# Performance work log

Hardware: AMD Instinct MI355X
Metric: run time of the kernel (lower is better)

The kernel has to match this reference:

```python
import jax, jax.numpy as jnp
import numpy as np

G = 20000   # total_genes = nodes per graph = output dim
HID = 64    # hidden_channels
H = 4       # attention heads (concat=False -> mean over heads)
E = 640000  # edges (avg degree 32)
B = 128     # batch of cell-line samples
PD = 600    # perturbation feature dim
NEG_SLOPE = 0.2


def _gat(x, edge_index, W, a_src, a_dst, b, heads):
    """PyG GATConv with add_self_loops=True, concat=False (head mean)."""
    N = x.shape[0]
    C = W.shape[1] // heads
    h = (x @ W).reshape(N, heads, C)              # [N,H,C]
    loop = jnp.arange(N, dtype=edge_index.dtype)
    src = jnp.concatenate([edge_index[0], loop])  # [E+N]
    dst = jnp.concatenate([edge_index[1], loop])
    e_src = jnp.sum(h * a_src[None], axis=-1)     # [N,H]
    e_dst = jnp.sum(h * a_dst[None], axis=-1)
    e = jax.nn.leaky_relu(e_src[src] + e_dst[dst], NEG_SLOPE)  # [E+N,H]
    # segment softmax over incoming edges of each target node
    m = jax.ops.segment_max(e, dst, num_segments=N)
    ex = jnp.exp(e - m[dst])
    denom = jax.ops.segment_sum(ex, dst, num_segments=N)
    alpha = ex / denom[dst]                        # [E+N,H]
    out = jax.ops.segment_sum(h[src] * alpha[:, :, None], dst, num_segments=N)
    return out.mean(axis=1) + b                    # concat=False -> mean heads


def _mlp(x, W1, b1, W2, b2):
    # MLP([a,b,c], 'Sigmoid'): Linear -> Sigmoid -> Linear (last act dropped)
    return jax.nn.sigmoid(x @ W1 + b1) @ W2 + b2


def setup_inputs() -> dict:
    key = jax.random.key(0)
    ks = jax.random.split(key, 26)
    s = 0.05  # small init to keep sigmoids in their active range
    rn = lambda k, shp: jax.random.normal(k, shp, jnp.float32)
    return {
        "x": rn(ks[0], (G, 1)),
        "edge_index": jax.random.randint(ks[1], (2, E), 0, G, dtype=jnp.int32),
        "pos": jnp.arange(G, dtype=jnp.int32),
        "ctrl": rn(ks[2], (B, G)),
        "pert": rn(ks[3], (B, PD)),
        "gene_embed": rn(ks[4], (G, HID)) * s,
        "conv1_W": rn(ks[5], (1 + HID, H * HID)) * s,
        "conv1_as": rn(ks[6], (H, HID)) * s,
        "conv1_ad": rn(ks[7], (H, HID)) * s,
        "conv1_b": rn(ks[8], (HID,)) * s,
        "lin1_W": rn(ks[9], (1 + HID, HID)) * s,
        "lin1_b": rn(ks[10], (HID,)) * s,
        "conv2_W": rn(ks[11], (HID, H * 1)) * s,
        "conv2_as": rn(ks[12], (H, 1)) * s,
        "conv2_ad": rn(ks[13], (H, 1)) * s,
        "conv2_b": rn(ks[14], (1,)) * s,
        "lin2_W": rn(ks[15], (HID, 1)) * s,
        "lin2_b": rn(ks[16], (1,)) * s,
        "pert_W1": rn(ks[17], (PD, 128)) * s,
        "pert_b1": rn(ks[18], (128,)) * s,
        "pert_W2": rn(ks[19], (128, HID)) * s,
        "pert_b2": rn(ks[20], (HID,)) * s,
        "pred_W1": rn(ks[21], (G + HID, 1024)) * s,
        "pred_b1": rn(ks[22], (1024,)) * s,
        "pred_W2": rn(ks[23], (1024, G)) * s,
        "pred_b2": rn(ks[24], (G,)) * s,
    }


def reference(x, edge_index, pos, ctrl, pert, gene_embed,
              conv1_W, conv1_as, conv1_ad, conv1_b, lin1_W, lin1_b,
              conv2_W, conv2_as, conv2_ad, conv2_b, lin2_W, lin2_b,
              pert_W1, pert_b1, pert_W2, pert_b2,
              pred_W1, pred_b1, pred_W2, pred_b2):
    # per-graph GNN (single cell-type key), all_feat=True
    xc = jnp.concatenate([x, gene_embed[pos]], axis=1)         # [G, 1+HID]
    h1 = jax.nn.sigmoid(_gat(xc, edge_index, conv1_W, conv1_as, conv1_ad, conv1_b, H)
                        + xc @ lin1_W + lin1_b)                # [G, HID]
    h2 = jax.nn.sigmoid(_gat(h1, edge_index, conv2_W, conv2_as, conv2_ad, conv2_b, H)
                        + h1 @ lin2_W + lin2_b)                # [G, 1]
    feat = h2[:, 0]                                            # dense batch squeeze -> [G]
    # every sample in the batch uses this cell type's features
    z = feat[None, :] + ctrl                                   # [B, G]
    p = _mlp(pert, pert_W1, pert_b1, pert_W2, pert_b2)         # embd_pert -> [B, HID]
    inp = jnp.concatenate([z, p], axis=1)                      # [B, G+HID]
    return _mlp(inp, pred_W1, pred_b1, pred_W2, pred_b2)       # [B, G]
```

## Files before the change

kernel.cpp:

```cpp
#include <hip/hip_runtime.h>
#include <math.h>

#define G 20000
#define E_EDGES 640000
#define HID 64
#define NHEAD 4
#define BATCH 128
#define PD 600
#define NEG 0.2f
#define MAXN 128

#define KA1 20096
#define NSTEP1 628
#define KSPLIT1 32
#define KA2 1024

#define ROWS_HC 16

typedef float v4f __attribute__((ext_vector_type(4)));
typedef short short8 __attribute__((ext_vector_type(8)));

__device__ __forceinline__ float sigmoidf_(float x){ return 1.0f/(1.0f+__expf(-x)); }
__device__ __forceinline__ float leakyf_(float x){ return x>=0.f ? x : NEG*x; }
__device__ __forceinline__ unsigned short f2bf(float f){
    unsigned int u = __float_as_uint(f);
    return (unsigned short)((u + 0x7FFFu + ((u >> 16) & 1u)) >> 16);
}
__device__ __forceinline__ float bf2f(unsigned short b){
    return __uint_as_float(((unsigned int)b) << 16);
}

__global__ __launch_bounds__(320)
void k_hc(const float* __restrict__ x, const int* __restrict__ pos,
          const float* __restrict__ ge, const float* __restrict__ Wc,
          const float* __restrict__ Wl, const float* __restrict__ as_,
          const float* __restrict__ ad_,
          unsigned short* __restrict__ hcb, float* __restrict__ hlin,
          float* __restrict__ es, float* __restrict__ ed)
{
    int t = threadIdx.x;
    int rb = blockIdx.x * ROWS_HC;
    __shared__ float xc[ROWS_HC][68];
    for (int l = t; l < ROWS_HC*65; l += 320){
        int r = l / 65, k = l - r*65;
        int row = rb + r;
        float v = 0.f;
        if (row < G) v = (k == 0) ? x[row] : ge[pos[row]*HID + (k-1)];
        xc[r][k] = v;
    }
    float wcol[65];
    if (t < 256){
        #pragma unroll
        for (int k = 0; k < 65; ++k) wcol[k] = Wc[k*256 + t];
    } else {
        int c = t - 256;
        #pragma unroll
        for (int k = 0; k < 65; ++k) wcol[k] = Wl[k*64 + c];
    }
    float a_s = 0.f, a_d = 0.f;
    if (t < 256){ a_s = as_[t]; a_d = ad_[t]; }
    __syncthreads();

    int nrow = G - rb; if (nrow > ROWS_HC) nrow = ROWS_HC;
    for (int r = 0; r < nrow; ++r){
        int row = rb + r;
        const float4* xr = (const float4*)&xc[r][0];
        float b0 = 0.f, b1 = 0.f, b2 = 0.f, b3 = 0.f;
        #pragma unroll
        for (int k4 = 0; k4 < 16; ++k4){
            float4 v = xr[k4];
            b0 += v.x*wcol[4*k4];
            b1 += v.y*wcol[4*k4+1];
            b2 += v.z*wcol[4*k4+2];
            b3 += v.w*wcol[4*k4+3];
        }
        float acc = (b0 + b1) + (b2 + b3) + xc[r][64] * wcol[64];
        if (t < 256){
            hcb[(size_t)row*256 + t] = f2bf(acc);
            float v1 = acc * a_s, v2 = acc * a_d;
            #pragma unroll
            for (int m = 32; m; m >>= 1){ v1 += __shfl_xor(v1, m); v2 += __shfl_xor(v2, m); }
            if ((t & 63) == 0){ int h = t >> 6; es[row*4+h] = v1; ed[row*4+h] = v2; }
        } else {
            hlin[(size_t)row*64 + (t - 256)] = acc;
        }
    }
}

__global__ void k_hist(const int* __restrict__ ei, int* __restrict__ cnt){
    int e = blockIdx.x*blockDim.x + threadIdx.x;
    if (e < E_EDGES) atomicAdd(&cnt[ei[E_EDGES + e]], 1);
}
__global__ void k_scan(const int* __restrict__ cnt, int* __restrict__ offs,
                       int* __restrict__ cur)
{
    __shared__ int ts[1024];
    int t = threadIdx.x;
    int base = t * 20;
    int loc[20];
    int s = 0;
    #pragma unroll
    for (int j = 0; j < 20; ++j){
        int i = base + j;
        int v = (i < G) ? cnt[i] : 0;
        loc[j] = s; s += v;
    }
    ts[t] = s;
    __syncthreads();
    for (int off = 1; off < 1024; off <<= 1){
        int add = (t >= off) ? ts[t - off] : 0;
        __syncthreads();
        ts[t] += add;
        __syncthreads();
    }
    int tb = (t == 0) ? 0 : ts[t - 1];
    #pragma unroll
    for (int j = 0; j < 20; ++j){
        int i = base + j;
        if (i < G){ int o = tb + loc[j]; offs[i] = o; cur[i] = o; }
    }
    if (t == 0) offs[G] = ts[1023];
}
__global__ void k_scatter(const int* __restrict__ ei, int* __restrict__ cur, int* __restrict__ csr){
    int e = blockIdx.x*blockDim.x + threadIdx.x;
    if (e < E_EDGES){
        int d = ei[E_EDGES + e];
        int p = atomicAdd(&cur[d], 1);
        csr[p] = ei[e];
    }
}

__global__ __launch_bounds__(256)
void k_gat1(const unsigned short* __restrict__ hcb, const float* __restrict__ hlin,
            const float* __restrict__ es, const float* __restrict__ ed,
            const int* __restrict__ offs, const int* __restrict__ csr,
            const float* __restrict__ bc1, const float* __restrict__ bl1,
            const float* __restrict__ W2c, const float* __restrict__ as2,
            const float* __restrict__ ad2, const float* __restrict__ Wl2,
            float* __restrict__ hh2, float* __restrict__ es2o,
            float* __restrict__ ed2o, float* __restrict__ lv)
{
    int t = threadIdx.x;
    int lane = t & 63, wv = t >> 6;
    int d = blockIdx.x * 4 + wv;
    __shared__ float4 wcache[4][MAXN];
    __shared__ int    wsrc[4][MAXN];
    int o = offs[d];
    int deg = offs[d+1] - o;
    int total = deg + 1;
    if (total > MAXN) total = MAXN;
    float4 edv = *(const float4*)(ed + d*4);

    float s0x=-1e30f, s0y=-1e30f, s0z=-1e30f, s0w=-1e30f;
    float s1x=-1e30f, s1y=-1e30f, s1z=-1e30f, s1w=-1e30f;
    if (lane < total){
        int s = (lane < deg) ? csr[o + lane] : d;
        wsrc[wv][lane] = s;
        float4 ev = *(const float4*)(es + s*4);
        s0x = leakyf_(ev.x + edv.x); s0y = leakyf_(ev.y + edv.y);
        s0z = leakyf_(ev.z + edv.z); s0w = leakyf_(ev.w + edv.w);
    }
    int i1 = lane + 64;
    if (i1 < total){
        int s = (i1 < deg) ? csr[o + i1] : d;
        wsrc[wv][i1] = s;
        float4 ev = *(const float4*)(es + s*4);
        s1x = leakyf_(ev.x + edv.x); s1y = leakyf_(ev.y + edv.y);
        s1z = leakyf_(ev.z + edv.z); s1w = leakyf_(ev.w + edv.w);
    }
    float m0 = fmaxf(s0x, s1x), m1 = fmaxf(s0y, s1y);
    float m2 = fmaxf(s0z, s1z), m3 = fmaxf(s0w, s1w);
    #pragma unroll
    for (int m = 32; m; m >>= 1){
        m0 = fmaxf(m0, __shfl_xor(m0, m)); m1 = fmaxf(m1, __shfl_xor(m1, m));
        m2 = fmaxf(m2, __shfl_xor(m2, m)); m3 = fmaxf(m3, __shfl_xor(m3, m));
    }
    float e0x = __expf(s0x - m0), e0y = __expf(s0y - m1);
    float e0z = __expf(s0z - m2), e0w = __expf(s0w - m3);
    float e1x = __expf(s1x - m0), e1y = __expf(s1y - m1);
    float e1z = __expf(s1z - m2), e1w = __expf(s1w - m3);
    float q0 = e0x + e1x, q1 = e0y + e1y, q2 = e0z + e1z, q3 = e0w + e1w;
    #pragma unroll
    for (int m = 32; m; m >>= 1){
        q0 += __shfl_xor(q0, m); q1 += __shfl_xor(q1, m);
        q2 += __shfl_xor(q2, m); q3 += __shfl_xor(q3, m);
    }
    float inv0 = 1.0f/q0, inv1 = 1.0f/q1, inv2 = 1.0f/q2, inv3 = 1.0f/q3;
    if (lane < total) wcache[wv][lane] = make_float4(e0x*inv0, e0y*inv1, e0z*inv2, e0w*inv3);
    if (i1   < total) wcache[wv][i1]   = make_float4(e1x*inv0, e1y*inv1, e1z*inv2, e1w*inv3);
    __syncthreads();

    int u = lane;
    int h = u >> 4;
    float a0=0.f, a1=0.f, a2=0.f, a3=0.f;
    uint2 v; float al;
    {
        int s = wsrc[wv][0];
        al = ((const float*)&wcache[wv][0])[h];
        v = *(const uint2*)(hcb + (size_t)s*256 + u*4);
    }
    for (int idx = 0; idx < total; ){
        uint2 vc = v; float ac = al;
        int nx = idx + 1;
        if (nx < total){
            int s2 = wsrc[wv][nx];
            al = ((const float*)&wcache[wv][nx])[h];
            v = *(const uint2*)(hcb + (size_t)s2*256 + u*4);
        }
        a0 += ac * __uint_as_float(vc.x << 16);
        a1 += ac * __uint_as_float(vc.x & 0xFFFF0000u);
        a2 += ac * __uint_as_float(vc.y << 16);
        a3 += ac * __uint_as_float(vc.y & 0xFFFF0000u);
        idx = nx;
    }
    a0 += __shfl_xor(a0, 16); a1 += __shfl_xor(a1, 16);
    a2 += __shfl_xor(a2, 16); a3 += __shfl_xor(a3, 16);
    a0 += __shfl_xor(a0, 32); a1 += __shfl_xor(a1, 32);
    a2 += __shfl_xor(a2, 32); a3 += __shfl_xor(a3, 32);

    int cb = (lane & 15) * 4;
    float4 hl  = *(const float4*)(hlin + (size_t)d*64 + cb);
    float4 bcv = *(const float4*)(bc1 + cb);
    float4 blv = *(const float4*)(bl1 + cb);
    float h0 = sigmoidf_(0.25f*a0 + bcv.x + hl.x + blv.x);
    float h1v= sigmoidf_(0.25f*a1 + bcv.y + hl.y + blv.y);
    float h2v= sigmoidf_(0.25f*a2 + bcv.z + hl.z + blv.z);
    float h3v= sigmoidf_(0.25f*a3 + bcv.w + hl.w + blv.w);
    float p0 = h0*W2c[cb*4+0] + h1v*W2c[(cb+1)*4+0] + h2v*W2c[(cb+2)*4+0] + h3v*W2c[(cb+3)*4+0];
    float p1 = h0*W2c[cb*4+1] + h1v*W2c[(cb+1)*4+1] + h2v*W2c[(cb+2)*4+1] + h3v*W2c[(cb+3)*4+1];
    float p2 = h0*W2c[cb*4+2] + h1v*W2c[(cb+1)*4+2] + h2v*W2c[(cb+2)*4+2] + h3v*W2c[(cb+3)*4+2];
    float p3 = h0*W2c[cb*4+3] + h1v*W2c[(cb+1)*4+3] + h2v*W2c[(cb+2)*4+3] + h3v*W2c[(cb+3)*4+3];
    float pl = h0*Wl2[cb] + h1v*Wl2[cb+1] + h2v*Wl2[cb+2] + h3v*Wl2[cb+3];
    #pragma unroll
    for (int m = 1; m <= 8; m <<= 1){
        p0 += __shfl_xor(p0, m); p1 += __shfl_xor(p1, m);
        p2 += __shfl_xor(p2, m); p3 += __shfl_xor(p3, m);
        pl += __shfl_xor(pl, m);
    }
    if (lane == 0){
        hh2[d*4+0] = p0; hh2[d*4+1] = p1; hh2[d*4+2] = p2; hh2[d*4+3] = p3;
        es2o[d*4+0] = p0*as2[0]; es2o[d*4+1] = p1*as2[1];
        es2o[d*4+2] = p2*as2[2]; es2o[d*4+3] = p3*as2[3];
        ed2o[d*4+0] = p0*ad2[0]; ed2o[d*4+1] = p1*ad2[1];
        ed2o[d*4+2] = p2*ad2[2]; ed2o[d*4+3] = p3*ad2[3];
        lv[d] = pl;
    }
}

__global__ void k_gat2(const float* __restrict__ hh2, const float* __restrict__ es2,
                       const float* __restrict__ ed2, const int* __restrict__ offs,
                       const int* __restrict__ csr, const float* __restrict__ lv,
                       const float* __restrict__ bc2, const float* __restrict__ bl2,
                       float* __restrict__ feat)
{
    int d = blockIdx.x; int j = threadIdx.x;
    int o = offs[d];
    int deg = offs[d+1] - o;
    int total = deg + 1;
    float edst[4];
    #pragma unroll
    for (int h = 0; h < 4; ++h) edst[h] = ed2[d*4+h];
    float lmax[4] = {-1e30f,-1e30f,-1e30f,-1e30f};
    for (int idx = j; idx < total; idx += 64){
        int s = (idx < deg) ? csr[o + idx] : d;
        #pragma unroll
        for (int h = 0; h < 4; ++h)
            lmax[h] = fmaxf(lmax[h], leakyf_(es2[s*4+h] + edst[h]));
    }
    #pragma unroll
    for (int h = 0; h < 4; ++h)
        for (int m = 32; m; m >>= 1) lmax[h] = fmaxf(lmax[h], __shfl_xor(lmax[h], m));
    float lsum[4] = {0.f,0.f,0.f,0.f};
    float lnum[4] = {0.f,0.f,0.f,0.f};
    for (int idx = j; idx < total; idx += 64){
        int s = (idx < deg) ? csr[o + idx] : d;
        #pragma unroll
        for (int h = 0; h < 4; ++h){
            float e  = leakyf_(es2[s*4+h] + edst[h]);
            float ex = __expf(e - lmax[h]);
            lsum[h] += ex;
            lnum[h] += ex * hh2[s*4+h];
        }
    }
    #pragma unroll
    for (int h = 0; h < 4; ++h){
        for (int m = 32; m; m >>= 1){ lsum[h] += __shfl_xor(lsum[h], m); lnum[h] += __shfl_xor(lnum[h], m); }
    }
    if (j == 0){
        float sum = 0.f;
        #pragma unroll
        for (int h = 0; h < 4; ++h) sum += lnum[h] / lsum[h];
        feat[d] = sigmoidf_(0.25f*sum + bc2[0] + lv[d] + bl2[0]);
    }
}

__global__ void k_prepA(const float* __restrict__ ctrl, const float* __restrict__ feat,
                        unsigned short* __restrict__ Abf)
{
    int col = blockIdx.x*256 + threadIdx.x;
    int row = blockIdx.y;
    if (col < 20000)
        Abf[(size_t)row*KA1 + col] = f2bf(ctrl[(size_t)row*20000 + col] + feat[col]);
}

__global__ void k_pert(const float* __restrict__ pert, const float* __restrict__ W1,
                       const float* __restrict__ b1, const float* __restrict__ W2,
                       const float* __restrict__ b2, unsigned short* __restrict__ Abf)
{
    int r = blockIdx.x; int t = threadIdx.x;
    __shared__ float hid[128];
    float acc = 0.f;
    for (int k = 0; k < PD; ++k) acc += pert[r*PD + k] * W1[k*128 + t];
    hid[t] = sigmoidf_(acc + b1[t]);
    __syncthreads();
    if (t < 64){
        float a2 = 0.f;
        for (int k = 0; k < 128; ++k) a2 += hid[k] * W2[k*64 + t];
        Abf[(size_t)r*KA1 + 20000 + t] = f2bf(a2 + b2[t]);
    } else if (t < 96){
        Abf[(size_t)r*KA1 + 20000 + t] = 0;
    }
}

__global__ __launch_bounds__(256, 2)
void k_gemm1m(const unsigned short* __restrict__ Abf, const float* __restrict__ W1,
              float* __restrict__ part)
{
    int t = threadIdx.x;
    int lane = t & 63, wv = t >> 6;
    int lane16 = lane & 15, quad = lane >> 4, quad8 = quad * 8;
    int colbase = blockIdx.x * 64;
    int ks = blockIdx.y;
    int sbeg = (ks * NSTEP1) / KSPLIT1;
    int send = ((ks + 1) * NSTEP1) / KSPLIT1;
    int nsteps = send - sbeg;
    int kbeg = sbeg * 32;
    __shared__ unsigned short Bs[2][32*64];

    v4f acc[8];
    #pragma unroll
    for (int i = 0; i < 8; ++i) acc[i] = (v4f){0.f,0.f,0.f,0.f};

    int krow = t >> 3;
    int ng   = (t & 7) * 8;
    {
        int kg = kbeg + krow;
        short8 p;
        if (kg < 20064){
            float4 a = *(const float4*)(W1 + (size_t)kg*1024 + colbase + ng);
            float4 b = *(const float4*)(W1 + (size_t)kg*1024 + colbase + ng + 4);
            p[0]=(short)f2bf(a.x); p[1]=(short)f2bf(a.y); p[2]=(short)f2bf(a.z); p[3]=(short)f2bf(a.w);
            p[4]=(short)f2bf(b.x); p[5]=(short)f2bf(b.y); p[6]=(short)f2bf(b.z); p[7]=(short)f2bf(b.w);
        } else {
            p = (short8){0,0,0,0,0,0,0,0};
        }
        *(short8*)&Bs[0][krow*64 + ng] = p;
    }
    __syncthreads();

    int cur = 0;
    for (int s = 0; s < nsteps; ++s){
        int kg = kbeg + s*32;
        short8 bfrag;
        #pragma unroll
        for (int j = 0; j < 8; ++j)
            bfrag[j] = (short)Bs[cur][(quad8 + j)*64 + wv*16 + lane16];
        float w[8];
        bool more = (s + 1) < nsteps;
        if (more){
            int kn = kg + 32 + krow;
            if (kn < 20064){
                float4 a = *(const float4*)(W1 + (size_t)kn*1024 + colbase + ng);
                float4 b = *(const float4*)(W1 + (size_t)kn*1024 + colbase + ng + 4);
                w[0]=a.x; w[1]=a.y; w[2]=a.z; w[3]=a.w; w[4]=b.x; w[5]=b.y; w[6]=b.z; w[7]=b.w;
            } else {
                #pragma unroll
                for (int i = 0; i < 8; ++i) w[i] = 0.f;
            }
        }
        #pragma unroll
        for (int mt = 0; mt < 8; ++mt){
            short8 af = *(const short8*)(Abf + (size_t)(mt*16 + lane16)*KA1 + kg + quad8);
            acc[mt] = __builtin_amdgcn_mfma_f32_16x16x32_bf16(af, bfrag, acc[mt], 0, 0, 0);
        }
        if (more){
            short8 p;
            #pragma unroll
            for (int i = 0; i < 8; ++i) p[i] = (short)f2bf(w[i]);
            *(short8*)&Bs[cur^1][krow*64 + ng] = p;
        }
        __syncthreads();
        cur ^= 1;
    }
    float* dst = part + (size_t)ks * 131072;
    int col = colbase + wv*16 + lane16;
    #pragma unroll
    for (int mt = 0; mt < 8; ++mt)
        #pragma unroll
        for (int r = 0; r < 4; ++r)
            dst[(size_t)(mt*16 + quad*4 + r)*1024 + col] = acc[mt][r];
}

__global__ void k_reduce(const float* __restrict__ part, const float* __restrict__ b1,
                         unsigned short* __restrict__ hidbf)
{
    int row = blockIdx.x;
    int col = blockIdx.y*256 + threadIdx.x;
    float s = 0.f;
    #pragma unroll
    for (int ks = 0; ks < KSPLIT1; ++ks)
        s += part[(size_t)ks*131072 + (size_t)row*1024 + col];
    hidbf[(size_t)row*1024 + col] = f2bf(sigmoidf_(s + b1[col]));
}

__global__ __launch_bounds__(256, 2)
void k_gemm2m(const unsigned short* __restrict__ hidbf, const float* __restrict__ W2,
              const float* __restrict__ b2, float* __restrict__ out)
{
    int t = threadIdx.x;
    int lane = t & 63, wv = t >> 6;
    int lane16 = lane & 15, quad = lane >> 4, quad8 = quad * 8;
    int colbase = blockIdx.x * 64;
    int rbase   = blockIdx.y * 64;
    __shared__ unsigned short Bs[2][32*64];

    v4f acc[4];
    #pragma unroll
    for (int i = 0; i < 4; ++i) acc[i] = (v4f){0.f,0.f,0.f,0.f};

    int krow = t >> 3;
    int ng   = (t & 7) * 8;
    bool cv = (colbase + ng) < 20000;
    {
        short8 p = (short8){0,0,0,0,0,0,0,0};
        if (cv){
            float4 a = *(const float4*)(W2 + (size_t)krow*20000 + colbase + ng);
            float4 b = *(const float4*)(W2 + (size_t)krow*20000 + colbase + ng + 4);
            p[0]=(short)f2bf(a.x); p[1]=(short)f2bf(a.y); p[2]=(short)f2bf(a.z); p[3]=(short)f2bf(a.w);
            p[4]=(short)f2bf(b.x); p[5]=(short)f2bf(b.y); p[6]=(short)f2bf(b.z); p[7]=(short)f2bf(b.w);
        }
        *(short8*)&Bs[0][krow*64 + ng] = p;
    }
    __syncthreads();

    int cur = 0;
    for (int s = 0; s < 32; ++s){
        int kg = s*32;
        short8 bfrag;
        #pragma unroll
        for (int j = 0; j < 8; ++j)
            bfrag[j] = (short)Bs[cur][(quad8 + j)*64 + wv*16 + lane16];
        float w[8];
        bool more = s < 31;
        if (more){
            if (cv){
                int kn = kg + 32 + krow;
                float4 a = *(const float4*)(W2 + (size_t)kn*20000 + colbase + ng);
                float4 b = *(const float4*)(W2 + (size_t)kn*20000 + colbase + ng + 4);
                w[0]=a.x; w[1]=a.y; w[2]=a.z; w[3]=a.w; w[4]=b.x; w[5]=b.y; w[6]=b.z; w[7]=b.w;
            } else {
                #pragma unroll
                for (int i = 0; i < 8; ++i) w[i] = 0.f;
            }
        }
        #pragma unroll
        for (int mt = 0; mt < 4; ++mt){
            short8 af = *(const short8*)(hidbf + (size_t)(rbase + mt*16 + lane16)*KA2 + kg + quad8);
            acc[mt] = __builtin_amdgcn_mfma_f32_16x16x32_bf16(af, bfrag, acc[mt], 0, 0, 0);
        }
        if (more){
            short8 p;
            #pragma unroll
            for (int i = 0; i < 8; ++i) p[i] = (short)f2bf(w[i]);
            *(short8*)&Bs[cur^1][krow*64 + ng] = p;
        }
        __syncthreads();
        cur ^= 1;
    }
    int col = colbase + wv*16 + lane16;
    if (col < 20000){
        float bb = b2[col];
        #pragma unroll
        for (int mt = 0; mt < 4; ++mt)
            #pragma unroll
            for (int r = 0; r < 4; ++r)
                out[(size_t)(rbase + mt*16 + quad*4 + r)*20000 + col] = acc[mt][r] + bb;
    }
}

extern "C" void kernel_launch(void* const* d_in, const int* in_sizes, int n_in,
                              void* d_out, int out_size, void* d_ws, size_t ws_size,
                              hipStream_t stream)
{
    const float* x    = (const float*)d_in[0];
    const int*   ei   = (const int*)  d_in[1];
    const int*   pos  = (const int*)  d_in[2];
    const float* ctrl = (const float*)d_in[3];
    const float* pert = (const float*)d_in[4];
    const float* ge   = (const float*)d_in[5];
    const float* c1W  = (const float*)d_in[6];
    const float* c1as = (const float*)d_in[7];
    const float* c1ad = (const float*)d_in[8];
    const float* c1b  = (const float*)d_in[9];
    const float* l1W  = (const float*)d_in[10];
    const float* l1b  = (const float*)d_in[11];
    const float* c2W  = (const float*)d_in[12];
    const float* c2as = (const float*)d_in[13];
    const float* c2ad = (const float*)d_in[14];
    const float* c2b  = (const float*)d_in[15];
    const float* l2W  = (const float*)d_in[16];
    const float* l2b  = (const float*)d_in[17];
    const float* pW1  = (const float*)d_in[18];
    const float* pb1  = (const float*)d_in[19];
    const float* pW2  = (const float*)d_in[20];
    const float* pb2  = (const float*)d_in[21];
    const float* prW1 = (const float*)d_in[22];
    const float* prb1 = (const float*)d_in[23];
    const float* prW2 = (const float*)d_in[24];
    const float* prb2 = (const float*)d_in[25];
    float* out = (float*)d_out;

    char* ws = (char*)d_ws;
    size_t off = 0;
    auto alloc = [&](size_t bytes)->void*{
        void* pp = ws + off;
        off += (bytes + 255) & ~(size_t)255;
        return pp;
    };
    unsigned short* hcb  = (unsigned short*)alloc((size_t)G*256*2);
    float* hlin = (float*)alloc((size_t)G*64*4);
    float* es1  = (float*)alloc((size_t)G*4*4);
    float* ed1  = (float*)alloc((size_t)G*4*4);
    float* hh2  = (float*)alloc((size_t)G*4*4);
    float* es2  = (float*)alloc((size_t)G*4*4);
    float* ed2  = (float*)alloc((size_t)G*4*4);
    float* lv   = (float*)alloc((size_t)G*4);
    float* feat = (float*)alloc((size_t)G*4);
    unsigned short* hidbf = (unsigned short*)alloc((size_t)128*KA2*2);
    unsigned short* Abf1  = (unsigned short*)alloc((size_t)128*KA1*2);
    float* part = (float*)alloc((size_t)KSPLIT1*131072*4);
    int*   cnt  = (int*)alloc((size_t)G*4);
    int*   offs = (int*)alloc((size_t)(G+1)*4);
    int*   cur  = (int*)alloc((size_t)G*4);
    int*   csr  = (int*)alloc((size_t)E_EDGES*4);

    hipMemsetAsync(cnt, 0, (size_t)G*4, stream);

    k_hist   <<<(E_EDGES+255)/256, 256, 0, stream>>>(ei, cnt);
    k_scan   <<<1, 1024, 0, stream>>>(cnt, offs, cur);
    k_scatter<<<(E_EDGES+255)/256, 256, 0, stream>>>(ei, cur, csr);

    k_hc   <<<(G + ROWS_HC - 1)/ROWS_HC, 320, 0, stream>>>(x, pos, ge, c1W, l1W, c1as, c1ad,
                                         hcb, hlin, es1, ed1);
    k_gat1 <<<G/4, 256, 0, stream>>>(hcb, hlin, es1, ed1, offs, csr, c1b, l1b,
                                     c2W, c2as, c2ad, l2W, hh2, es2, ed2, lv);
    k_gat2 <<<G, 64, 0, stream>>>(hh2, es2, ed2, offs, csr, lv, c2b, l2b, feat);

    dim3 gp(79, 128);
    k_prepA<<<gp, 256, 0, stream>>>(ctrl, feat, Abf1);
    k_pert <<<BATCH, 128, 0, stream>>>(pert, pW1, pb1, pW2, pb2, Abf1);

    dim3 g1(16, KSPLIT1);
    k_gemm1m<<<g1, 256, 0, stream>>>(Abf1, prW1, part);
    dim3 gr(128, 4);
    k_reduce<<<gr, 256, 0, stream>>>(part, prb1, hidbf);
    dim3 g2(313, 2);
    k_gemm2m<<<g2, 256, 0, stream>>>(hidbf, prW2, prb2, out);
}
```

Before: 595.2 us.

## Split-K the second predictor GEMM and swizzle its LDS tile

The second predictor GEMM (128x1024 by 1024x20000) is split along K into four slices across a 626x4 grid, each writing fp32 partials that a new reduce kernel sums and then adds the bias. The grid is also reorganised so the two row halves sharing a column tile are adjacent in blockIdx.x, which may improve L2 reuse of W2. The LDS B tile gets an XOR swizzle to reduce bank conflicts on the column-strided fragment reads. The cost is about 40 MB of extra partial-sum write and read traffic and one more launch, in exchange for more blocks and shorter per-block K loops.

```diff
diff --git a/kernel.cpp b/kernel.cpp
--- a/kernel.cpp
+++ b/kernel.cpp
@@ -14,6 +14,8 @@
 #define NSTEP1 628
 #define KSPLIT1 32
 #define KA2 1024
+#define KSPLIT2 4
+#define P2STRIDE 2560000
 
 #define ROWS_HC 16
 
@@ -415,13 +417,15 @@
 
 __global__ __launch_bounds__(256, 2)
 void k_gemm2m(const unsigned short* __restrict__ hidbf, const float* __restrict__ W2,
-              const float* __restrict__ b2, float* __restrict__ out)
+              float* __restrict__ part2)
 {
     int t = threadIdx.x;
     int lane = t & 63, wv = t >> 6;
     int lane16 = lane & 15, quad = lane >> 4, quad8 = quad * 8;
-    int colbase = blockIdx.x * 64;
-    int rbase   = blockIdx.y * 64;
+    int colbase = (blockIdx.x >> 1) * 64;
+    int rbase   = (blockIdx.x & 1) * 64;
+    int ks      = blockIdx.y;
+    int kbeg    = ks * 256;
     __shared__ unsigned short Bs[2][32*64];
 
     v4f acc[4];
@@ -430,28 +434,31 @@
 
     int krow = t >> 3;
     int ng   = (t & 7) * 8;
+    int wng  = ng ^ ((krow >> 3) << 4);
     bool cv = (colbase + ng) < 20000;
     {
         short8 p = (short8){0,0,0,0,0,0,0,0};
         if (cv){
-            float4 a = *(const float4*)(W2 + (size_t)krow*20000 + colbase + ng);
-            float4 b = *(const float4*)(W2 + (size_t)krow*20000 + colbase + ng + 4);
+            int kg = kbeg + krow;
+            float4 a = *(const float4*)(W2 + (size_t)kg*20000 + colbase + ng);
+            float4 b = *(const float4*)(W2 + (size_t)kg*20000 + colbase + ng + 4);
             p[0]=(short)f2bf(a.x); p[1]=(short)f2bf(a.y); p[2]=(short)f2bf(a.z); p[3]=(short)f2bf(a.w);
             p[4]=(short)f2bf(b.x); p[5]=(short)f2bf(b.y); p[6]=(short)f2bf(b.z); p[7]=(short)f2bf(b.w);
         }
-        *(short8*)&Bs[0][krow*64 + ng] = p;
+        *(short8*)&Bs[0][krow*64 + wng] = p;
     }
     __syncthreads();
 
+    int swcol = (wv*16 + lane16) ^ (quad << 4);
     int cur = 0;
-    for (int s = 0; s < 32; ++s){
-        int kg = s*32;
+    for (int s = 0; s < 8; ++s){
+        int kg = kbeg + s*32;
         short8 bfrag;
         #pragma unroll
         for (int j = 0; j < 8; ++j)
-            bfrag[j] = (short)Bs[cur][(quad8 + j)*64 + wv*16 + lane16];
+            bfrag[j] = (short)Bs[cur][(quad8 + j)*64 + swcol];
         float w[8];
-        bool more = s < 31;
+        bool more = s < 7;
         if (more){
             if (cv){
                 int kn = kg + 32 + krow;
@@ -472,19 +479,33 @@
             short8 p;
             #pragma unroll
             for (int i = 0; i < 8; ++i) p[i] = (short)f2bf(w[i]);
-            *(short8*)&Bs[cur^1][krow*64 + ng] = p;
+            *(short8*)&Bs[cur^1][krow*64 + wng] = p;
         }
         __syncthreads();
         cur ^= 1;
     }
+    float* dst = part2 + (size_t)ks * P2STRIDE;
     int col = colbase + wv*16 + lane16;
     if (col < 20000){
-        float bb = b2[col];
         #pragma unroll
         for (int mt = 0; mt < 4; ++mt)
             #pragma unroll
             for (int r = 0; r < 4; ++r)
-                out[(size_t)(rbase + mt*16 + quad*4 + r)*20000 + col] = acc[mt][r] + bb;
+                dst[(size_t)(rbase + mt*16 + quad*4 + r)*20000 + col] = acc[mt][r];
+    }
+}
+
+__global__ void k_reduce2(const float* __restrict__ part2, const float* __restrict__ b2,
+                          float* __restrict__ out)
+{
+    int row = blockIdx.x;
+    int col = blockIdx.y*256 + threadIdx.x;
+    if (col < 20000){
+        float s = 0.f;
+        #pragma unroll
+        for (int ks = 0; ks < KSPLIT2; ++ks)
+            s += part2[(size_t)ks*P2STRIDE + (size_t)row*20000 + col];
+        out[(size_t)row*20000 + col] = s + b2[col];
     }
 }
 
@@ -538,7 +559,8 @@
     float* feat = (float*)alloc((size_t)G*4);
     unsigned short* hidbf = (unsigned short*)alloc((size_t)128*KA2*2);
     unsigned short* Abf1  = (unsigned short*)alloc((size_t)128*KA1*2);
-    float* part = (float*)alloc((size_t)KSPLIT1*131072*4);
+    float* part = (float*)alloc((size_t)KSPLIT2*P2STRIDE*4);
+    float* part2 = part;
     int*   cnt  = (int*)alloc((size_t)G*4);
     int*   offs = (int*)alloc((size_t)(G+1)*4);
     int*   cur  = (int*)alloc((size_t)G*4);
@@ -564,6 +586,8 @@
     k_gemm1m<<<g1, 256, 0, stream>>>(Abf1, prW1, part);
     dim3 gr(128, 4);
     k_reduce<<<gr, 256, 0, stream>>>(part, prb1, hidbf);
-    dim3 g2(313, 2);
-    k_gemm2m<<<g2, 256, 0, stream>>>(hidbf, prW2, prb2, out);
-}
+    dim3 g2(626, KSPLIT2);
+    k_gemm2m<<<g2, 256, 0, stream>>>(hidbf, prW2, part2);
+    dim3 gr2(128, 79);
+    k_reduce2<<<gr2, 256, 0, stream>>>(part2, prb2, out);
+}
```

Measured after the change: 590.7 us. Within noise of the previous version (-0.7%).
